# Performance work log

Hardware: AMD Instinct MI355X
Metric: run time of the kernel (lower is better)

The kernel has to match this reference:

```python
import jax, jax.numpy as jnp
import numpy as np

N = 100000   # nodes
E = 1600000  # edges
D_IN = 128
D = 128
G = 64       # graphs in batch
C = 2        # out_channels
EPS = 1e-5   # BatchNorm eps


def setup_inputs() -> dict:
    key = jax.random.key(0)
    ks = jax.random.split(key, 24)
    s = 0.05
    inp = {
        "x": jax.random.normal(ks[0], (N, D_IN), dtype=jnp.float32),
        "edge_index": jax.random.randint(ks[1], (2, E), 0, N, dtype=jnp.int32),
        "edge_attr": jax.random.uniform(ks[2], (E, 2), dtype=jnp.float32),
        "batch": jnp.sort(jax.random.randint(ks[3], (N,), 0, G, dtype=jnp.int32)),
        # GCN layer 0
        "Wg0": jax.random.normal(ks[4], (D_IN, D), dtype=jnp.float32) * s,
        "bg0": jnp.zeros((D,), jnp.float32),
        "gamma0": jnp.ones((D,), jnp.float32),
        "beta0": jnp.zeros((D,), jnp.float32),
        # GCN layer 1
        "Wg1": jax.random.normal(ks[5], (D, D), dtype=jnp.float32) * s,
        "bg1": jnp.zeros((D,), jnp.float32),
        "gamma1": jnp.ones((D,), jnp.float32),
        "beta1": jnp.zeros((D,), jnp.float32),
        # dense head
        "Wl1": jax.random.normal(ks[6], (D, D), dtype=jnp.float32) * s,
        "bl1": jnp.zeros((D,), jnp.float32),
        "Wl2": jax.random.normal(ks[7], (D, D), dtype=jnp.float32) * s,
        "bl2": jnp.zeros((D,), jnp.float32),
        "Wc1": jax.random.normal(ks[8], (D, D), dtype=jnp.float32) * s,
        "bc1": jnp.zeros((D,), jnp.float32),
        "Wc2": jax.random.normal(ks[9], (D, C), dtype=jnp.float32) * s,
        "bc2": jnp.zeros((C,), jnp.float32),
    }
    return inp


def _gcn_conv(x, src, dst, w, W, b):
    # PyG GCNConv: h = x @ W ; add self-loops (weight 1) ; symmetric norm ; agg at dst ; + bias
    h = x @ W                                                   # [N, D]
    deg = jax.ops.segment_sum(w, dst, num_segments=N) + 1.0     # self-loop weight 1
    dinv = jnp.where(deg > 0, jax.lax.rsqrt(deg), 0.0)          # deg^{-1/2}
    norm = dinv[src] * w * dinv[dst]                            # [E]
    agg = jax.ops.segment_sum(norm[:, None] * h[src], dst, num_segments=N)
    agg = agg + (dinv * dinv)[:, None] * h                      # self-loop contribution
    return agg + b


def _bn(x, gamma, beta):
    # training-mode batch statistics over the node dimension
    m = x.mean(axis=0)
    v = x.var(axis=0)
    return (x - m) * jax.lax.rsqrt(v + EPS) * gamma + beta


def reference(x, edge_index, edge_attr, batch,
              Wg0, bg0, gamma0, beta0,
              Wg1, bg1, gamma1, beta1,
              Wl1, bl1, Wl2, bl2, Wc1, bc1, Wc2, bc2):
    src, dst = edge_index[0], edge_index[1]
    w = edge_attr[:, 1]  # which_edge_weight is None -> column 1

    h = jax.nn.relu(_gcn_conv(x, src, dst, w, Wg0, bg0))
    h = _bn(h, gamma0, beta0)                 # dropout: identity (eval)
    h = jax.nn.relu(_gcn_conv(h, src, dst, w, Wg1, bg1))
    h = _bn(h, gamma1, beta1)

    h = jax.nn.relu(h @ Wl1 + bl1)
    h = h @ Wl2 + bl2                          # node embeddings [N, D]

    counts = jax.ops.segment_sum(jnp.ones((N,), h.dtype), batch, num_segments=G)
    graph_reps = jax.ops.segment_sum(h, batch, num_segments=G) / jnp.maximum(counts, 1.0)[:, None]

    logits = jax.nn.relu(graph_reps @ Wc1 + bc1) @ Wc2 + bc2   # [G, C]
    return (h, graph_reps, logits)
```

## Files before the change

### kernel.cpp

```cpp
#include <hip/hip_runtime.h>

#define N_NODES 100000
#define N_EDGES 1600000
#define DFEAT   128
#define NGRAPH  64
#define EPSV    1e-5f
#define SCAN_BLOCKS ((N_NODES + 255) / 256)
#define DEG_SCALE 268435456.0f
#define DEG_MASK  ((1ULL << 42) - 1)

typedef float v4f  __attribute__((ext_vector_type(4)));
typedef short v8s  __attribute__((ext_vector_type(8)));
typedef unsigned short us4 __attribute__((ext_vector_type(4)));
typedef unsigned short us8 __attribute__((ext_vector_type(8)));

static __device__ __forceinline__ unsigned short f2bf(float f) {
    union { float f; unsigned int u; } v; v.f = f;
    unsigned int u = v.u;
    return (unsigned short)((u + 0x7FFFu + ((u >> 16) & 1u)) >> 16);
}
static __device__ __forceinline__ float bf2f(unsigned short b) {
    union { unsigned int u; float f; } v; v.u = ((unsigned int)b) << 16;
    return v.f;
}

__global__ void init_kernel(unsigned long long* __restrict__ degcnt,
                            int* __restrict__ fillc, float* __restrict__ stats0,
                            float* __restrict__ stats1, float* __restrict__ gsum,
                            float* __restrict__ gcntf) {
    int i = blockIdx.x * 256 + threadIdx.x;
    if (i < N_NODES) { degcnt[i] = 0ULL; fillc[i] = 0; }
    if (i < 256)  { stats0[i] = 0.f; stats1[i] = 0.f; }
    if (i < NGRAPH * DFEAT) gsum[i] = 0.f;
    if (i < NGRAPH) gcntf[i] = 0.f;
}

__global__ __launch_bounds__(256) void wprep_kernel(
    const float* __restrict__ W0, const float* __restrict__ W1,
    const float* __restrict__ W2, const float* __restrict__ W3,
    unsigned short* __restrict__ T0, unsigned short* __restrict__ T1,
    unsigned short* __restrict__ T2, unsigned short* __restrict__ T3) {
    int which = blockIdx.x >> 6;
    int i = (blockIdx.x & 63) * 256 + threadIdx.x;
    const float* W = which == 0 ? W0 : which == 1 ? W1 : which == 2 ? W2 : W3;
    unsigned short* T = which == 0 ? T0 : which == 1 ? T1 : which == 2 ? T2 : T3;
    int n = i >> 7, k = i & 127;
    T[n * 128 + k] = f2bf(W[k * 128 + n]);
}

__global__ void edge_degcnt_kernel(const int* __restrict__ ei, const float* __restrict__ ea,
                                   unsigned long long* __restrict__ degcnt) {
    int e = blockIdx.x * 256 + threadIdx.x;
    if (e >= N_EDGES) return;
    int d = ei[N_EDGES + e];
    float w = ea[2 * e + 1];
    unsigned long long v = (1ULL << 42) | (unsigned long long)(w * DEG_SCALE);
    atomicAdd(&degcnt[d], v);
}

__global__ void dinv_kernel(const unsigned long long* __restrict__ degcnt,
                            int* __restrict__ cnt, float* __restrict__ dinv) {
    int i = blockIdx.x * 256 + threadIdx.x;
    if (i >= N_NODES) return;
    unsigned long long u = degcnt[i];
    cnt[i] = (int)(u >> 42);
    float deg = 1.0f + (float)(u & DEG_MASK) * (1.0f / DEG_SCALE);
    dinv[i] = rsqrtf(deg);
}

__global__ __launch_bounds__(256) void scan1_kernel(const int* __restrict__ cnt,
                                                    int* __restrict__ blockSum) {
    __shared__ int lds[256];
    int i = blockIdx.x * 256 + threadIdx.x;
    int t = threadIdx.x;
    lds[t] = (i < N_NODES) ? cnt[i] : 0;
    __syncthreads();
    for (int off = 128; off > 0; off >>= 1) {
        if (t < off) lds[t] += lds[t + off];
        __syncthreads();
    }
    if (t == 0) blockSum[blockIdx.x] = lds[0];
}

__global__ __launch_bounds__(512) void scan2_kernel(int* __restrict__ blockSum) {
    __shared__ int lds[512];
    int t = threadIdx.x;
    int v = (t < SCAN_BLOCKS) ? blockSum[t] : 0;
    lds[t] = v;
    __syncthreads();
    for (int off = 1; off < 512; off <<= 1) {
        int u = (t >= off) ? lds[t - off] : 0;
        __syncthreads();
        lds[t] += u;
        __syncthreads();
    }
    if (t < SCAN_BLOCKS) blockSum[t] = lds[t] - v;
}

__global__ __launch_bounds__(256) void scan3_kernel(const int* __restrict__ cnt,
                                                    const int* __restrict__ blockSum,
                                                    int* __restrict__ rowptr) {
    __shared__ int lds[256];
    int i = blockIdx.x * 256 + threadIdx.x;
    int t = threadIdx.x;
    int v = (i < N_NODES) ? cnt[i] : 0;
    lds[t] = v;
    __syncthreads();
    for (int off = 1; off < 256; off <<= 1) {
        int u = (t >= off) ? lds[t - off] : 0;
        __syncthreads();
        lds[t] += u;
        __syncthreads();
    }
    if (i < N_NODES) rowptr[i] = blockSum[blockIdx.x] + lds[t] - v;
    if (i == 0) rowptr[N_NODES] = N_EDGES;
}

__global__ void fill_kernel(const int* __restrict__ ei, const float* __restrict__ ea,
                            const float* __restrict__ dinv, const int* __restrict__ rowptr,
                            int* __restrict__ fillc, int2* __restrict__ edges) {
    int e = blockIdx.x * 256 + threadIdx.x;
    if (e >= N_EDGES) return;
    int s = ei[e], d = ei[N_EDGES + e];
    float w = ea[2 * e + 1];
    float nrm = dinv[s] * w * dinv[d];
    int pos = rowptr[d] + atomicAdd(&fillc[d], 1);
    edges[pos] = make_int2(s, __float_as_int(nrm));
}

__global__ __launch_bounds__(256) void gemm_bf16_kernel(
    const void* __restrict__ Xv, int x_is_f32,
    const unsigned short* __restrict__ Wt,
    void* __restrict__ Outv, int out_is_f32,
    const float* __restrict__ bnp, const float* __restrict__ bias, int do_relu) {
    __shared__ unsigned short Xs[128][136];
    __shared__ unsigned short Ws[128][136];
    const int tid = threadIdx.x;
    const int rb = blockIdx.x * 128;

#pragma unroll
    for (int it = 0; it < 8; ++it) {
        int flat = it * 2048 + tid * 8;
        int n = flat >> 7, k = flat & 127;
        *(us8*)&Ws[n][k] = *(const us8*)&Wt[n * 128 + k];
    }
    if (x_is_f32) {
        const float* X = (const float*)Xv;
#pragma unroll
        for (int it = 0; it < 16; ++it) {
            int flat = it * 1024 + tid * 4;
            int r = flat >> 7, k = flat & 127;
            float4 v = make_float4(0.f, 0.f, 0.f, 0.f);
            if (rb + r < N_NODES) v = *(const float4*)&X[(size_t)(rb + r) * 128 + k];
            if (bnp) {
                v.x = v.x * bnp[k]     + bnp[128 + k];
                v.y = v.y * bnp[k + 1] + bnp[129 + k];
                v.z = v.z * bnp[k + 2] + bnp[130 + k];
                v.w = v.w * bnp[k + 3] + bnp[131 + k];
            }
            us4 o; o.x = f2bf(v.x); o.y = f2bf(v.y); o.z = f2bf(v.z); o.w = f2bf(v.w);
            *(us4*)&Xs[r][k] = o;
        }
    } else {
        const unsigned short* X = (const unsigned short*)Xv;
#pragma unroll
        for (int it = 0; it < 8; ++it) {
            int flat = it * 2048 + tid * 8;
            int r = flat >> 7, k = flat & 127;
            us8 v = {0, 0, 0, 0, 0, 0, 0, 0};
            if (rb + r < N_NODES) v = *(const us8*)&X[(size_t)(rb + r) * 128 + k];
            if (bnp) {
#pragma unroll
                for (int j = 0; j < 8; ++j)
                    v[j] = f2bf(bf2f(v[j]) * bnp[k + j] + bnp[128 + k + j]);
            }
            *(us8*)&Xs[r][k] = v;
        }
    }
    __syncthreads();

    const int wv = tid >> 6, lane = tid & 63;
    const int q = lane >> 4, c16 = lane & 15;
    v4f acc[2][8];
#pragma unroll
    for (int i = 0; i < 2; ++i)
#pragma unroll
        for (int j = 0; j < 8; ++j) acc[i][j] = (v4f){0.f, 0.f, 0.f, 0.f};

#pragma unroll
    for (int ks = 0; ks < 4; ++ks) {
        v8s a0 = *(const v8s*)&Xs[wv * 32 + c16][ks * 32 + q * 8];
        v8s a1 = *(const v8s*)&Xs[wv * 32 + 16 + c16][ks * 32 + q * 8];
#pragma unroll
        for (int nt = 0; nt < 8; ++nt) {
            v8s b = *(const v8s*)&Ws[nt * 16 + c16][ks * 32 + q * 8];
            acc[0][nt] = __builtin_amdgcn_mfma_f32_16x16x32_bf16(a0, b, acc[0][nt], 0, 0, 0);
            acc[1][nt] = __builtin_amdgcn_mfma_f32_16x16x32_bf16(a1, b, acc[1][nt], 0, 0, 0);
        }
    }

#pragma unroll
    for (int mt = 0; mt < 2; ++mt) {
#pragma unroll
        for (int nt = 0; nt < 8; ++nt) {
            int col = nt * 16 + c16;
            float bcol = bias ? bias[col] : 0.f;
#pragma unroll
            for (int r = 0; r < 4; ++r) {
                int row = rb + wv * 32 + mt * 16 + q * 4 + r;
                if (row >= N_NODES) continue;
                float o = acc[mt][nt][r] + bcol;
                if (do_relu) o = fmaxf(o, 0.f);
                if (out_is_f32) ((float*)Outv)[(size_t)row * 128 + col] = o;
                else ((unsigned short*)Outv)[(size_t)row * 128 + col] = f2bf(o);
            }
        }
    }
}

__global__ __launch_bounds__(256) void agg_relu_bf16_kernel(
    const unsigned short* __restrict__ H, const int* __restrict__ rowptr,
    const int2* __restrict__ edges,
    const float* __restrict__ dinv, const float* __restrict__ bias,
    unsigned short* __restrict__ outb, float* __restrict__ stats, int nwaves) {
    __shared__ float red[1024];
    const int tid = threadIdx.x;
    const int wv = tid >> 6;
    const int lane = tid & 63;
    const float bx = bias[2 * lane], by = bias[2 * lane + 1];
    const unsigned int* __restrict__ H4 = (const unsigned int*)H;
    unsigned int* __restrict__ O4 = (unsigned int*)outb;
    float s0 = 0.f, q0 = 0.f, s1 = 0.f, q1 = 0.f;

    for (int i = blockIdx.x * 4 + wv; i < N_NODES; i += nwaves) {
        int beg = __builtin_amdgcn_readfirstlane(rowptr[i]);
        int end = __builtin_amdgcn_readfirstlane(rowptr[i + 1]);
        float di = dinv[i];
        unsigned int hs = H4[(size_t)i * 64 + lane];
        float px0 = 0.f, py0 = 0.f, px1 = 0.f, py1 = 0.f;
        float px2 = 0.f, py2 = 0.f, px3 = 0.f, py3 = 0.f;
        const int last = end - 1;
        for (int j = beg; j < end; j += 8) {
            int j1 = j + 1 < end ? j + 1 : last;
            int j2 = j + 2 < end ? j + 2 : last;
            int j3 = j + 3 < end ? j + 3 : last;
            int j4 = j + 4 < end ? j + 4 : last;
            int j5 = j + 5 < end ? j + 5 : last;
            int j6 = j + 6 < end ? j + 6 : last;
            int j7 = j + 7 < end ? j + 7 : last;
            int2 e0 = edges[j];
            int2 e1 = edges[j1];
            int2 e2 = edges[j2];
            int2 e3 = edges[j3];
            int2 e4 = edges[j4];
            int2 e5 = edges[j5];
            int2 e6 = edges[j6];
            int2 e7 = edges[j7];
            unsigned int h0 = H4[(size_t)e0.x * 64 + lane];
            unsigned int h1 = H4[(size_t)e1.x * 64 + lane];
            unsigned int h2 = H4[(size_t)e2.x * 64 + lane];
            unsigned int h3 = H4[(size_t)e3.x * 64 + lane];
            unsigned int h4 = H4[(size_t)e4.x * 64 + lane];
            unsigned int h5 = H4[(size_t)e5.x * 64 + lane];
            unsigned int h6 = H4[(size_t)e6.x * 64 + lane];
            unsigned int h7 = H4[(size_t)e7.x * 64 + lane];
            float v0 = __int_as_float(e0.y);
            float v1 = j + 1 < end ? __int_as_float(e1.y) : 0.f;
            float v2 = j + 2 < end ? __int_as_float(e2.y) : 0.f;
            float v3 = j + 3 < end ? __int_as_float(e3.y) : 0.f;
            float v4 = j + 4 < end ? __int_as_float(e4.y) : 0.f;
            float v5 = j + 5 < end ? __int_as_float(e5.y) : 0.f;
            float v6 = j + 6 < end ? __int_as_float(e6.y) : 0.f;
            float v7 = j + 7 < end ? __int_as_float(e7.y) : 0.f;
            px0 = fmaf(v0, bf2f((unsigned short)h0), px0);
            py0 = fmaf(v0, bf2f((unsigned short)(h0 >> 16)), py0);
            px1 = fmaf(v1, bf2f((unsigned short)h1), px1);
            py1 = fmaf(v1, bf2f((unsigned short)(h1 >> 16)), py1);
            px2 = fmaf(v2, bf2f((unsigned short)h2), px2);
            py2 = fmaf(v2, bf2f((unsigned short)(h2 >> 16)), py2);
            px3 = fmaf(v3, bf2f((unsigned short)h3), px3);
            py3 = fmaf(v3, bf2f((unsigned short)(h3 >> 16)), py3);
            px0 = fmaf(v4, bf2f((unsigned short)h4), px0);
            py0 = fmaf(v4, bf2f((unsigned short)(h4 >> 16)), py0);
            px1 = fmaf(v5, bf2f((unsigned short)h5), px1);
            py1 = fmaf(v5, bf2f((unsigned short)(h5 >> 16)), py1);
            px2 = fmaf(v6, bf2f((unsigned short)h6), px2);
            py2 = fmaf(v6, bf2f((unsigned short)(h6 >> 16)), py2);
            px3 = fmaf(v7, bf2f((unsigned short)h7), px3);
            py3 = fmaf(v7, bf2f((unsigned short)(h7 >> 16)), py3);
        }
        float dd = di * di;
        float ax = (px0 + px1) + (px2 + px3);
        float ay = (py0 + py1) + (py2 + py3);
        ax = fmaf(dd, bf2f((unsigned short)hs), ax) + bx;
        ay = fmaf(dd, bf2f((unsigned short)(hs >> 16)), ay) + by;
        ax = fmaxf(ax, 0.f);
        ay = fmaxf(ay, 0.f);
        O4[(size_t)i * 64 + lane] =
            (unsigned int)f2bf(ax) | ((unsigned int)f2bf(ay) << 16);
        s0 += ax; q0 += ax * ax; s1 += ay; q1 += ay * ay;
    }

    red[wv * 128 + 2 * lane]           = s0;
    red[wv * 128 + 2 * lane + 1]       = s1;
    red[512 + wv * 128 + 2 * lane]     = q0;
    red[512 + wv * 128 + 2 * lane + 1] = q1;
    __syncthreads();
    if (tid < 128) {
        float ts = red[tid] + red[128 + tid] + red[256 + tid] + red[384 + tid];
        float tq = red[512 + tid] + red[640 + tid] + red[768 + tid] + red[896 + tid];
        atomicAdd(&stats[tid], ts);
        atomicAdd(&stats[128 + tid], tq);
    }
}

__global__ void bn_finalize_kernel(const float* __restrict__ stats,
                                   const float* __restrict__ gamma,
                                   const float* __restrict__ beta,
                                   float* __restrict__ bnp) {
    int f = threadIdx.x;
    float mean = stats[f] / (float)N_NODES;
    float var = stats[128 + f] / (float)N_NODES - mean * mean;
    float sc = gamma[f] * rsqrtf(var + EPSV);
    bnp[f] = sc;
    bnp[128 + f] = beta[f] - mean * sc;
}

__global__ __launch_bounds__(256) void pool_kernel(const float* __restrict__ h,
                                                   const int* __restrict__ batch,
                                                   float* __restrict__ gsum,
                                                   float* __restrict__ gcntf) {
    const int f = threadIdx.x & 127;
    const int half = threadIdx.x >> 7;
    const int base = blockIdx.x * 128;
    int r = base + half;
    const int end = (base + 128 < N_NODES) ? base + 128 : N_NODES;
    if (r >= end) return;
    int cur = batch[r];
    float sum = 0.f, cnt = 0.f;
    for (; r < end; r += 2) {
        int g = batch[r];
        if (g != cur) {
            atomicAdd(&gsum[cur * 128 + f], sum);
            if (f == 0) atomicAdd(&gcntf[cur], cnt);
            sum = 0.f; cnt = 0.f; cur = g;
        }
        sum += h[(size_t)r * 128 + f];
        cnt += 1.f;
    }
    atomicAdd(&gsum[cur * 128 + f], sum);
    if (f == 0) atomicAdd(&gcntf[cur], cnt);
}

__global__ void reps_kernel(const float* __restrict__ gsum,
                            const float* __restrict__ gcntf,
                            float* __restrict__ out_reps) {
    int i = blockIdx.x * 256 + threadIdx.x;
    if (i < NGRAPH * 128) {
        int g = i >> 7;
        out_reps[i] = gsum[i] / fmaxf(gcntf[g], 1.0f);
    }
}

__global__ __launch_bounds__(128) void logits_kernel(
    const float* __restrict__ reps, const float* __restrict__ Wc1,
    const float* __restrict__ bc1, const float* __restrict__ Wc2,
    const float* __restrict__ bc2, float* __restrict__ out_logits) {
    __shared__ float repS[128];
    __shared__ float tmp[128];
    int g = blockIdx.x, t = threadIdx.x;
    repS[t] = reps[(size_t)g * 128 + t];
    __syncthreads();
    float acc = bc1[t];
    for (int k = 0; k < 128; ++k) acc = fmaf(repS[k], Wc1[k * 128 + t], acc);
    tmp[t] = fmaxf(acc, 0.f);
    __syncthreads();
    if (t < 2) {
        float a = bc2[t];
        for (int k = 0; k < 128; ++k) a = fmaf(tmp[k], Wc2[k * 2 + t], a);
        out_logits[g * 2 + t] = a;
    }
}

extern "C" void kernel_launch(void* const* d_in, const int* in_sizes, int n_in,
                              void* d_out, int out_size, void* d_ws, size_t ws_size,
                              hipStream_t stream) {
    const float* x      = (const float*)d_in[0];
    const int*   ei     = (const int*)d_in[1];
    const float* ea     = (const float*)d_in[2];
    const int*   batch  = (const int*)d_in[3];
    const float* Wg0    = (const float*)d_in[4];
    const float* bg0    = (const float*)d_in[5];
    const float* gamma0 = (const float*)d_in[6];
    const float* beta0  = (const float*)d_in[7];
    const float* Wg1    = (const float*)d_in[8];
    const float* bg1    = (const float*)d_in[9];
    const float* gamma1 = (const float*)d_in[10];
    const float* beta1  = (const float*)d_in[11];
    const float* Wl1    = (const float*)d_in[12];
    const float* bl1    = (const float*)d_in[13];
    const float* Wl2    = (const float*)d_in[14];
    const float* bl2    = (const float*)d_in[15];
    const float* Wc1    = (const float*)d_in[16];
    const float* bc1    = (const float*)d_in[17];
    const float* Wc2    = (const float*)d_in[18];
    const float* bc2    = (const float*)d_in[19];

    float* out = (float*)d_out;
    char* ws = (char*)d_ws;
    size_t off = 0;
    auto alloc = [&](size_t bytes) {
        void* p = ws + off;
        off += (bytes + 15) & ~(size_t)15;
        return p;
    };
    unsigned short* bufHb = (unsigned short*)alloc(sizeof(unsigned short) * (size_t)N_NODES * 128);
    unsigned short* bufAb = (unsigned short*)alloc(sizeof(unsigned short) * (size_t)N_NODES * 128);
    int2* edges = (int2*)alloc(sizeof(int2) * (size_t)N_EDGES);
    unsigned long long* degcnt = (unsigned long long*)alloc(sizeof(unsigned long long) * N_NODES);
    unsigned short* Wt0   = (unsigned short*)alloc(sizeof(unsigned short) * 128 * 128);
    unsigned short* Wt1   = (unsigned short*)alloc(sizeof(unsigned short) * 128 * 128);
    unsigned short* Wt2   = (unsigned short*)alloc(sizeof(unsigned short) * 128 * 128);
    unsigned short* Wt3   = (unsigned short*)alloc(sizeof(unsigned short) * 128 * 128);
    float* dinv   = (float*)alloc(sizeof(float) * N_NODES);
    int*   cnt    = (int*)alloc(sizeof(int) * N_NODES);
    int*   fillc  = (int*)alloc(sizeof(int) * N_NODES);
    float* stats0 = (float*)alloc(sizeof(float) * 256);
    float* stats1 = (float*)alloc(sizeof(float) * 256);
    float* bnp0   = (float*)alloc(sizeof(float) * 256);
    float* bnp1   = (float*)alloc(sizeof(float) * 256);
    float* gsum   = (float*)alloc(sizeof(float) * NGRAPH * 128);
    float* gcntf  = (float*)alloc(sizeof(float) * NGRAPH);
    int*   rowptr = (int*)alloc(sizeof(int) * (N_NODES + 1));
    int*   blockSum = (int*)alloc(sizeof(int) * SCAN_BLOCKS);

    init_kernel<<<(N_NODES + 255) / 256, 256, 0, stream>>>(degcnt, fillc, stats0,
                                                           stats1, gsum, gcntf);
    wprep_kernel<<<256, 256, 0, stream>>>(Wg0, Wg1, Wl1, Wl2, Wt0, Wt1, Wt2, Wt3);
    edge_degcnt_kernel<<<(N_EDGES + 255) / 256, 256, 0, stream>>>(ei, ea, degcnt);
    dinv_kernel<<<(N_NODES + 255) / 256, 256, 0, stream>>>(degcnt, cnt, dinv);
    scan1_kernel<<<SCAN_BLOCKS, 256, 0, stream>>>(cnt, blockSum);
    scan2_kernel<<<1, 512, 0, stream>>>(blockSum);
    scan3_kernel<<<SCAN_BLOCKS, 256, 0, stream>>>(cnt, blockSum, rowptr);
    fill_kernel<<<(N_EDGES + 255) / 256, 256, 0, stream>>>(ei, ea, dinv, rowptr, fillc,
                                                           edges);

    const int gemm_grid = (N_NODES + 127) / 128;
    const int agg_blocks = 2048;
    const int agg_nwaves = agg_blocks * 4;
    gemm_bf16_kernel<<<gemm_grid, 256, 0, stream>>>(x, 1, Wt0, bufHb, 0, nullptr, nullptr, 0);
    agg_relu_bf16_kernel<<<agg_blocks, 256, 0, stream>>>(bufHb, rowptr, edges,
                                                         dinv, bg0, bufAb, stats0, agg_nwaves);
    bn_finalize_kernel<<<1, 128, 0, stream>>>(stats0, gamma0, beta0, bnp0);
    gemm_bf16_kernel<<<gemm_grid, 256, 0, stream>>>(bufAb, 0, Wt1, bufHb, 0, bnp0, nullptr, 0);
    agg_relu_bf16_kernel<<<agg_blocks, 256, 0, stream>>>(bufHb, rowptr, edges,
                                                         dinv, bg1, bufAb, stats1, agg_nwaves);
    bn_finalize_kernel<<<1, 128, 0, stream>>>(stats1, gamma1, beta1, bnp1);
    gemm_bf16_kernel<<<gemm_grid, 256, 0, stream>>>(bufAb, 0, Wt2, bufHb, 0, bnp1, bl1, 1);
    gemm_bf16_kernel<<<gemm_grid, 256, 0, stream>>>(bufHb, 0, Wt3, out, 1, nullptr, bl2, 0);
    pool_kernel<<<(N_NODES + 127) / 128, 256, 0, stream>>>(out, batch, gsum, gcntf);
    reps_kernel<<<(NGRAPH * 128 + 255) / 256, 256, 0, stream>>>(
        gsum, gcntf, out + (size_t)N_NODES * 128);
    logits_kernel<<<NGRAPH, 128, 0, stream>>>(out + (size_t)N_NODES * 128, Wc1, bc1, Wc2,
                                              bc2, out + (size_t)N_NODES * 128 + NGRAPH * 128);
}
```

Before: 685.6 us.

## Fuse setup kernels, load GEMM A operand from global, fuse pooling into last GEMM

Merges init and weight-prep into one kernel, folds dinv computation into the first scan pass, and merges reps into the logits kernel, cutting several launches. The GEMM no longer stages X in shared memory: each lane loads its A fragment directly from global, which halves LDS use and allows launch_bounds occupancy 4. The final GEMM does mean-pool partial sums from registers and shared atomics, so the separate pool kernel and its re-read of the fp32 output are gone. In exchange, the direct loads are less coalesced, and the per-graph pooling loop adds barriers and atomics to that GEMM.

```diff
diff --git a/kernel.cpp b/kernel.cpp
--- a/kernel.cpp
+++ b/kernel.cpp
@@ -24,28 +24,28 @@
     return v.f;
 }
 
-__global__ void init_kernel(unsigned long long* __restrict__ degcnt,
-                            int* __restrict__ fillc, float* __restrict__ stats0,
-                            float* __restrict__ stats1, float* __restrict__ gsum,
-                            float* __restrict__ gcntf) {
-    int i = blockIdx.x * 256 + threadIdx.x;
+__global__ __launch_bounds__(256) void initprep_kernel(
+    unsigned long long* __restrict__ degcnt, int* __restrict__ fillc,
+    float* __restrict__ stats0, float* __restrict__ stats1,
+    float* __restrict__ gsum, float* __restrict__ gcntf,
+    const float* __restrict__ W0, const float* __restrict__ W1,
+    const float* __restrict__ W2, const float* __restrict__ W3,
+    unsigned short* __restrict__ T0, unsigned short* __restrict__ T1,
+    unsigned short* __restrict__ T2, unsigned short* __restrict__ T3) {
+    int bid = blockIdx.x;
+    int i = bid * 256 + threadIdx.x;
     if (i < N_NODES) { degcnt[i] = 0ULL; fillc[i] = 0; }
     if (i < 256)  { stats0[i] = 0.f; stats1[i] = 0.f; }
     if (i < NGRAPH * DFEAT) gsum[i] = 0.f;
     if (i < NGRAPH) gcntf[i] = 0.f;
-}
-
-__global__ __launch_bounds__(256) void wprep_kernel(
-    const float* __restrict__ W0, const float* __restrict__ W1,
-    const float* __restrict__ W2, const float* __restrict__ W3,
-    unsigned short* __restrict__ T0, unsigned short* __restrict__ T1,
-    unsigned short* __restrict__ T2, unsigned short* __restrict__ T3) {
-    int which = blockIdx.x >> 6;
-    int i = (blockIdx.x & 63) * 256 + threadIdx.x;
-    const float* W = which == 0 ? W0 : which == 1 ? W1 : which == 2 ? W2 : W3;
-    unsigned short* T = which == 0 ? T0 : which == 1 ? T1 : which == 2 ? T2 : T3;
-    int n = i >> 7, k = i & 127;
-    T[n * 128 + k] = f2bf(W[k * 128 + n]);
+    if (bid < 256) {
+        int which = bid >> 6;
+        int i2 = (bid & 63) * 256 + threadIdx.x;
+        const float* W = which == 0 ? W0 : which == 1 ? W1 : which == 2 ? W2 : W3;
+        unsigned short* T = which == 0 ? T0 : which == 1 ? T1 : which == 2 ? T2 : T3;
+        int n = i2 >> 7, k = i2 & 127;
+        T[n * 128 + k] = f2bf(W[k * 128 + n]);
+    }
 }
 
 __global__ void edge_degcnt_kernel(const int* __restrict__ ei, const float* __restrict__ ea,
@@ -58,22 +58,21 @@
     atomicAdd(&degcnt[d], v);
 }
 
-__global__ void dinv_kernel(const unsigned long long* __restrict__ degcnt,
-                            int* __restrict__ cnt, float* __restrict__ dinv) {
-    int i = blockIdx.x * 256 + threadIdx.x;
-    if (i >= N_NODES) return;
-    unsigned long long u = degcnt[i];
-    cnt[i] = (int)(u >> 42);
-    float deg = 1.0f + (float)(u & DEG_MASK) * (1.0f / DEG_SCALE);
-    dinv[i] = rsqrtf(deg);
-}
-
-__global__ __launch_bounds__(256) void scan1_kernel(const int* __restrict__ cnt,
-                                                    int* __restrict__ blockSum) {
+__global__ __launch_bounds__(256) void scan1d_kernel(
+    const unsigned long long* __restrict__ degcnt, int* __restrict__ cnt,
+    float* __restrict__ dinv, int* __restrict__ blockSum) {
     __shared__ int lds[256];
     int i = blockIdx.x * 256 + threadIdx.x;
     int t = threadIdx.x;
-    lds[t] = (i < N_NODES) ? cnt[i] : 0;
+    int c = 0;
+    if (i < N_NODES) {
+        unsigned long long u = degcnt[i];
+        c = (int)(u >> 42);
+        cnt[i] = c;
+        float deg = 1.0f + (float)(u & DEG_MASK) * (1.0f / DEG_SCALE);
+        dinv[i] = rsqrtf(deg);
+    }
+    lds[t] = c;
     __syncthreads();
     for (int off = 128; off > 0; off >>= 1) {
         if (t < off) lds[t] += lds[t + off];
@@ -128,12 +127,13 @@
     edges[pos] = make_int2(s, __float_as_int(nrm));
 }
 
-__global__ __launch_bounds__(256) void gemm_bf16_kernel(
+__global__ __launch_bounds__(256, 4) void gemm_bf16_kernel(
     const void* __restrict__ Xv, int x_is_f32,
     const unsigned short* __restrict__ Wt,
     void* __restrict__ Outv, int out_is_f32,
-    const float* __restrict__ bnp, const float* __restrict__ bias, int do_relu) {
-    __shared__ unsigned short Xs[128][136];
+    const float* __restrict__ bnp, const float* __restrict__ bias, int do_relu,
+    const int* __restrict__ batch, float* __restrict__ gsum,
+    float* __restrict__ gcntf, int do_pool) {
     __shared__ unsigned short Ws[128][136];
     const int tid = threadIdx.x;
     const int rb = blockIdx.x * 128;
@@ -144,43 +144,15 @@
         int n = flat >> 7, k = flat & 127;
         *(us8*)&Ws[n][k] = *(const us8*)&Wt[n * 128 + k];
     }
-    if (x_is_f32) {
-        const float* X = (const float*)Xv;
-#pragma unroll
-        for (int it = 0; it < 16; ++it) {
-            int flat = it * 1024 + tid * 4;
-            int r = flat >> 7, k = flat & 127;
-            float4 v = make_float4(0.f, 0.f, 0.f, 0.f);
-            if (rb + r < N_NODES) v = *(const float4*)&X[(size_t)(rb + r) * 128 + k];
-            if (bnp) {
-                v.x = v.x * bnp[k]     + bnp[128 + k];
-                v.y = v.y * bnp[k + 1] + bnp[129 + k];
-                v.z = v.z * bnp[k + 2] + bnp[130 + k];
-                v.w = v.w * bnp[k + 3] + bnp[131 + k];
-            }
-            us4 o; o.x = f2bf(v.x); o.y = f2bf(v.y); o.z = f2bf(v.z); o.w = f2bf(v.w);
-            *(us4*)&Xs[r][k] = o;
-        }
-    } else {
-        const unsigned short* X = (const unsigned short*)Xv;
-#pragma unroll
-        for (int it = 0; it < 8; ++it) {
-            int flat = it * 2048 + tid * 8;
-            int r = flat >> 7, k = flat & 127;
-            us8 v = {0, 0, 0, 0, 0, 0, 0, 0};
-            if (rb + r < N_NODES) v = *(const us8*)&X[(size_t)(rb + r) * 128 + k];
-            if (bnp) {
-#pragma unroll
-                for (int j = 0; j < 8; ++j)
-                    v[j] = f2bf(bf2f(v[j]) * bnp[k + j] + bnp[128 + k + j]);
-            }
-            *(us8*)&Xs[r][k] = v;
-        }
-    }
     __syncthreads();
 
     const int wv = tid >> 6, lane = tid & 63;
     const int q = lane >> 4, c16 = lane & 15;
+    const int rA = rb + wv * 32 + c16;
+    const int rB = rA + 16;
+    const size_t rAc = (size_t)(rA < N_NODES ? rA : N_NODES - 1);
+    const size_t rBc = (size_t)(rB < N_NODES ? rB : N_NODES - 1);
+
     v4f acc[2][8];
 #pragma unroll
     for (int i = 0; i < 2; ++i)
@@ -189,8 +161,62 @@
 
 #pragma unroll
     for (int ks = 0; ks < 4; ++ks) {
-        v8s a0 = *(const v8s*)&Xs[wv * 32 + c16][ks * 32 + q * 8];
-        v8s a1 = *(const v8s*)&Xs[wv * 32 + 16 + c16][ks * 32 + q * 8];
+        const int k0 = ks * 32 + q * 8;
+        v8s a0, a1;
+        if (x_is_f32) {
+            const float* X = (const float*)Xv;
+            float4 f0 = *(const float4*)&X[rAc * 128 + k0];
+            float4 f1 = *(const float4*)&X[rAc * 128 + k0 + 4];
+            float4 g0 = *(const float4*)&X[rBc * 128 + k0];
+            float4 g1 = *(const float4*)&X[rBc * 128 + k0 + 4];
+            if (bnp) {
+                float4 s0 = *(const float4*)&bnp[k0];
+                float4 s1 = *(const float4*)&bnp[k0 + 4];
+                float4 b0 = *(const float4*)&bnp[128 + k0];
+                float4 b1 = *(const float4*)&bnp[128 + k0 + 4];
+                f0.x = f0.x * s0.x + b0.x; f0.y = f0.y * s0.y + b0.y;
+                f0.z = f0.z * s0.z + b0.z; f0.w = f0.w * s0.w + b0.w;
+                f1.x = f1.x * s1.x + b1.x; f1.y = f1.y * s1.y + b1.y;
+                f1.z = f1.z * s1.z + b1.z; f1.w = f1.w * s1.w + b1.w;
+                g0.x = g0.x * s0.x + b0.x; g0.y = g0.y * s0.y + b0.y;
+                g0.z = g0.z * s0.z + b0.z; g0.w = g0.w * s0.w + b0.w;
+                g1.x = g1.x * s1.x + b1.x; g1.y = g1.y * s1.y + b1.y;
+                g1.z = g1.z * s1.z + b1.z; g1.w = g1.w * s1.w + b1.w;
+            }
+            us8 oa, ob;
+            oa[0] = f2bf(f0.x); oa[1] = f2bf(f0.y); oa[2] = f2bf(f0.z); oa[3] = f2bf(f0.w);
+            oa[4] = f2bf(f1.x); oa[5] = f2bf(f1.y); oa[6] = f2bf(f1.z); oa[7] = f2bf(f1.w);
+            ob[0] = f2bf(g0.x); ob[1] = f2bf(g0.y); ob[2] = f2bf(g0.z); ob[3] = f2bf(g0.w);
+            ob[4] = f2bf(g1.x); ob[5] = f2bf(g1.y); ob[6] = f2bf(g1.z); ob[7] = f2bf(g1.w);
+            a0 = *(v8s*)&oa; a1 = *(v8s*)&ob;
+        } else {
+            const unsigned short* X = (const unsigned short*)Xv;
+            us8 v0 = *(const us8*)&X[rAc * 128 + k0];
+            us8 v1 = *(const us8*)&X[rBc * 128 + k0];
+            if (bnp) {
+                float4 s0 = *(const float4*)&bnp[k0];
+                float4 s1 = *(const float4*)&bnp[k0 + 4];
+                float4 b0 = *(const float4*)&bnp[128 + k0];
+                float4 b1 = *(const float4*)&bnp[128 + k0 + 4];
+                v0[0] = f2bf(bf2f(v0[0]) * s0.x + b0.x);
+                v0[1] = f2bf(bf2f(v0[1]) * s0.y + b0.y);
+                v0[2] = f2bf(bf2f(v0[2]) * s0.z + b0.z);
+                v0[3] = f2bf(bf2f(v0[3]) * s0.w + b0.w);
+                v0[4] = f2bf(bf2f(v0[4]) * s1.x + b1.x);
+                v0[5] = f2bf(bf2f(v0[5]) * s1.y + b1.y);
+                v0[6] = f2bf(bf2f(v0[6]) * s1.z + b1.z);
+                v0[7] = f2bf(bf2f(v0[7]) * s1.w + b1.w);
+                v1[0] = f2bf(bf2f(v1[0]) * s0.x + b0.x);
+                v1[1] = f2bf(bf2f(v1[1]) * s0.y + b0.y);
+                v1[2] = f2bf(bf2f(v1[2]) * s0.z + b0.z);
+                v1[3] = f2bf(bf2f(v1[3]) * s0.w + b0.w);
+                v1[4] = f2bf(bf2f(v1[4]) * s1.x + b1.x);
+                v1[5] = f2bf(bf2f(v1[5]) * s1.y + b1.y);
+                v1[6] = f2bf(bf2f(v1[6]) * s1.z + b1.z);
+                v1[7] = f2bf(bf2f(v1[7]) * s1.w + b1.w);
+            }
+            a0 = *(v8s*)&v0; a1 = *(v8s*)&v1;
+        }
 #pragma unroll
         for (int nt = 0; nt < 8; ++nt) {
             v8s b = *(const v8s*)&Ws[nt * 16 + c16][ks * 32 + q * 8];
@@ -208,12 +234,56 @@
 #pragma unroll
             for (int r = 0; r < 4; ++r) {
                 int row = rb + wv * 32 + mt * 16 + q * 4 + r;
-                if (row >= N_NODES) continue;
                 float o = acc[mt][nt][r] + bcol;
                 if (do_relu) o = fmaxf(o, 0.f);
+                acc[mt][nt][r] = o;
+                if (row >= N_NODES) continue;
                 if (out_is_f32) ((float*)Outv)[(size_t)row * 128 + col] = o;
                 else ((unsigned short*)Outv)[(size_t)row * 128 + col] = f2bf(o);
             }
+        }
+    }
+
+    if (do_pool) {
+        __shared__ float pg[128];
+        __shared__ float pcnt;
+        int br[8];
+#pragma unroll
+        for (int mt = 0; mt < 2; ++mt)
+#pragma unroll
+            for (int r = 0; r < 4; ++r) {
+                int row = rb + wv * 32 + mt * 16 + q * 4 + r;
+                br[mt * 4 + r] = (row < N_NODES) ? batch[row] : -1;
+            }
+        int rlast = (rb + 127 < N_NODES) ? rb + 127 : N_NODES - 1;
+        int gmin = batch[rb];
+        int gmax = batch[rlast];
+        for (int g = gmin; g <= gmax; ++g) {
+            if (tid < 128) pg[tid] = 0.f;
+            if (tid == 0) pcnt = 0.f;
+            __syncthreads();
+            if (wv < 2) {
+                int rr = rb + tid;
+                bool p = (tid < 128) && (rr < N_NODES) && (batch[rr] == g);
+                unsigned long long m = __ballot(p);
+                if (lane == 0 && m) atomicAdd(&pcnt, (float)__popcll(m));
+            }
+#pragma unroll
+            for (int nt = 0; nt < 8; ++nt) {
+                float s = 0.f;
+#pragma unroll
+                for (int mt = 0; mt < 2; ++mt)
+#pragma unroll
+                    for (int r = 0; r < 4; ++r)
+                        if (br[mt * 4 + r] == g) s += acc[mt][nt][r];
+                s += __shfl_xor(s, 16);
+                s += __shfl_xor(s, 32);
+                if (q == 0 && s != 0.f) atomicAdd(&pg[nt * 16 + c16], s);
+            }
+            __syncthreads();
+            if (tid < 128 && pg[tid] != 0.f) atomicAdd(&gsum[g * 128 + tid], pg[tid]);
+            if (tid == 0 && pcnt != 0.f) atomicAdd(&gcntf[g], pcnt);
+            __syncthreads();
         }
     }
 }
@@ -326,50 +396,17 @@
     bnp[128 + f] = beta[f] - mean * sc;
 }
 
-__global__ __launch_bounds__(256) void pool_kernel(const float* __restrict__ h,
-                                                   const int* __restrict__ batch,
-                                                   float* __restrict__ gsum,
-                                                   float* __restrict__ gcntf) {
-    const int f = threadIdx.x & 127;
-    const int half = threadIdx.x >> 7;
-    const int base = blockIdx.x * 128;
-    int r = base + half;
-    const int end = (base + 128 < N_NODES) ? base + 128 : N_NODES;
-    if (r >= end) return;
-    int cur = batch[r];
-    float sum = 0.f, cnt = 0.f;
-    for (; r < end; r += 2) {
-        int g = batch[r];
-        if (g != cur) {
-            atomicAdd(&gsum[cur * 128 + f], sum);
-            if (f == 0) atomicAdd(&gcntf[cur], cnt);
-            sum = 0.f; cnt = 0.f; cur = g;
-        }
-        sum += h[(size_t)r * 128 + f];
-        cnt += 1.f;
-    }
-    atomicAdd(&gsum[cur * 128 + f], sum);
-    if (f == 0) atomicAdd(&gcntf[cur], cnt);
-}
-
-__global__ void reps_kernel(const float* __restrict__ gsum,
-                            const float* __restrict__ gcntf,
-                            float* __restrict__ out_reps) {
-    int i = blockIdx.x * 256 + threadIdx.x;
-    if (i < NGRAPH * 128) {
-        int g = i >> 7;
-        out_reps[i] = gsum[i] / fmaxf(gcntf[g], 1.0f);
-    }
-}
-
 __global__ __launch_bounds__(128) void logits_kernel(
-    const float* __restrict__ reps, const float* __restrict__ Wc1,
-    const float* __restrict__ bc1, const float* __restrict__ Wc2,
-    const float* __restrict__ bc2, float* __restrict__ out_logits) {
+    const float* __restrict__ gsum, const float* __restrict__ gcntf,
+    const float* __restrict__ Wc1, const float* __restrict__ bc1,
+    const float* __restrict__ Wc2, const float* __restrict__ bc2,
+    float* __restrict__ out_reps, float* __restrict__ out_logits) {
     __shared__ float repS[128];
     __shared__ float tmp[128];
     int g = blockIdx.x, t = threadIdx.x;
-    repS[t] = reps[(size_t)g * 128 + t];
+    float rep = gsum[(size_t)g * 128 + t] / fmaxf(gcntf[g], 1.0f);
+    out_reps[(size_t)g * 128 + t] = rep;
+    repS[t] = rep;
     __syncthreads();
     float acc = bc1[t];
     for (int k = 0; k < 128; ++k) acc = fmaf(repS[k], Wc1[k * 128 + t], acc);
@@ -434,12 +471,11 @@
     int*   rowptr = (int*)alloc(sizeof(int) * (N_NODES + 1));
     int*   blockSum = (int*)alloc(sizeof(int) * SCAN_BLOCKS);
 
-    init_kernel<<<(N_NODES + 255) / 256, 256, 0, stream>>>(degcnt, fillc, stats0,
-                                                           stats1, gsum, gcntf);
-    wprep_kernel<<<256, 256, 0, stream>>>(Wg0, Wg1, Wl1, Wl2, Wt0, Wt1, Wt2, Wt3);
+    initprep_kernel<<<SCAN_BLOCKS, 256, 0, stream>>>(degcnt, fillc, stats0, stats1,
+                                                     gsum, gcntf, Wg0, Wg1, Wl1, Wl2,
+                                                     Wt0, Wt1, Wt2, Wt3);
     edge_degcnt_kernel<<<(N_EDGES + 255) / 256, 256, 0, stream>>>(ei, ea, degcnt);
-    dinv_kernel<<<(N_NODES + 255) / 256, 256, 0, stream>>>(degcnt, cnt, dinv);
-    scan1_kernel<<<SCAN_BLOCKS, 256, 0, stream>>>(cnt, blockSum);
+    scan1d_kernel<<<SCAN_BLOCKS, 256, 0, stream>>>(degcnt, cnt, dinv, blockSum);
     scan2_kernel<<<1, 512, 0, stream>>>(blockSum);
     scan3_kernel<<<SCAN_BLOCKS, 256, 0, stream>>>(cnt, blockSum, rowptr);
     fill_kernel<<<(N_EDGES + 255) / 256, 256, 0, stream>>>(ei, ea, dinv, rowptr, fillc,
@@ -448,19 +484,21 @@
     const int gemm_grid = (N_NODES + 127) / 128;
     const int agg_blocks = 2048;
     const int agg_nwaves = agg_blocks * 4;
-    gemm_bf16_kernel<<<gemm_grid, 256, 0, stream>>>(x, 1, Wt0, bufHb, 0, nullptr, nullptr, 0);
+    gemm_bf16_kernel<<<gemm_grid, 256, 0, stream>>>(x, 1, Wt0, bufHb, 0, nullptr,
+                                                    nullptr, 0, nullptr, nullptr, nullptr, 0);
     agg_relu_bf16_kernel<<<agg_blocks, 256, 0, stream>>>(bufHb, rowptr, edges,
                                                          dinv, bg0, bufAb, stats0, agg_nwaves);
     bn_finalize_kernel<<<1, 128, 0, stream>>>(stats0, gamma0, beta0, bnp0);
-    gemm_bf16_kernel<<<gemm_grid, 256, 0, stream>>>(bufAb, 0, Wt1, bufHb, 0, bnp0, nullptr, 0);
+    gemm_bf16_kernel<<<gemm_grid, 256, 0, stream>>>(bufAb, 0, Wt1, bufHb, 0, bnp0,
+                                                    nullptr, 0, nullptr, nullptr, nullptr, 0);
     agg_relu_bf16_kernel<<<agg_blocks, 256, 0, stream>>>(bufHb, rowptr, edges,
                                                          dinv, bg1, bufAb, stats1, agg_nwaves);
     bn_finalize_kernel<<<1, 128, 0, stream>>>(stats1, gamma1, beta1, bnp1);
-    gemm_bf16_kernel<<<gemm_grid, 256, 0, stream>>>(bufAb, 0, Wt2, bufHb, 0, bnp1, bl1, 1);
-    gemm_bf16_kernel<<<gemm_grid, 256, 0, stream>>>(bufHb, 0, Wt3, out, 1, nullptr, bl2, 0);
-    pool_kernel<<<(N_NODES + 127) / 128, 256, 0, stream>>>(out, batch, gsum, gcntf);
-    reps_kernel<<<(NGRAPH * 128 + 255) / 256, 256, 0, stream>>>(
-        gsum, gcntf, out + (size_t)N_NODES * 128);
-    logits_kernel<<<NGRAPH, 128, 0, stream>>>(out + (size_t)N_NODES * 128, Wc1, bc1, Wc2,
-                                              bc2, out + (size_t)N_NODES * 128 + NGRAPH * 128);
-}
+    gemm_bf16_kernel<<<gemm_grid, 256, 0, stream>>>(bufAb, 0, Wt2, bufHb, 0, bnp1,
+                                                    bl1, 1, nullptr, nullptr, nullptr, 0);
+    gemm_bf16_kernel<<<gemm_grid, 256, 0, stream>>>(bufHb, 0, Wt3, out, 1, nullptr,
+                                                    bl2, 0, batch, gsum, gcntf, 1);
+    logits_kernel<<<NGRAPH, 128, 0, stream>>>(gsum, gcntf, Wc1, bc1, Wc2, bc2,
+                                              out + (size_t)N_NODES * 128,
+                                              out + (size_t)N_NODES * 128 + NGRAPH * 128);
+}
```

Result: faster. 584.0 us (-14.8%).
